# Kernel optimization log

Hardware: AMD Instinct MI355X
Metric: run time of the kernel (lower is better)

Reference implementation:

```python
import jax, jax.numpy as jnp
import numpy as np

S, B, I, H, O = 512, 64, 128, 512, 1


def setup_inputs() -> dict:
    key = jax.random.key(0)
    ks = jax.random.split(key, 12)
    s = 1.0 / np.sqrt(H)
    u = lambda k, shape: jax.random.uniform(k, shape, jnp.float32, -s, s)
    return {
        "inputs": jax.random.normal(ks[0], (S, B, I), jnp.float32),
        # pre nn.RNN (1 layer, tanh)
        "W_ih_pre": u(ks[1], (H, I)),
        "W_hh_pre": u(ks[2], (H, H)),
        "b_ih_pre": u(ks[3], (H,)),
        "b_hh_pre": u(ks[4], (H,)),
        # post nn.RNNCell (input_size=hidden_size)
        "W_ih_post": u(ks[5], (H, H)),
        "W_hh_post": u(ks[6], (H, H)),
        "b_ih_post": u(ks[7], (H,)),
        "b_hh_post": u(ks[8], (H,)),
        # fc head
        "W_fc": u(ks[9], (O, H)),
        "b_fc": u(ks[10], (O,)),
    }


def reference(inputs, W_ih_pre, W_hh_pre, b_ih_pre, b_hh_pre,
              W_ih_post, W_hh_post, b_ih_post, b_hh_post, W_fc, b_fc):
    batch = inputs.shape[1]
    hidden = W_ih_pre.shape[0]
    h0 = jnp.zeros((batch, hidden), inputs.dtype)

    # ---- pre RNN over time (tanh cell), inputs are (S, B, I) ----
    x_proj = jnp.einsum('sbi,hi->sbh', inputs, W_ih_pre) + b_ih_pre

    def pre_step(h, x_t):
        h = jnp.tanh(x_t + h @ W_hh_pre.T + b_hh_pre)
        return h, h

    _, out_pre = jax.lax.scan(pre_step, h0, x_proj)  # (S, B, H)

    # ---- attention loop: exactly `hidden` sequential steps ----
    def attn_step(h, _):
        # dot-prod alignment: sum over feature dim -> (S, B)
        scores = jnp.einsum('sbh,bh->sb', out_pre, h)
        w = jax.nn.softmax(scores, axis=0)          # softmax over seq dim
        ctx = jnp.einsum('sbh,sb->bh', out_pre, w)  # weighted sum -> (B, H)
        h = jnp.tanh(ctx @ W_ih_post.T + b_ih_post + h @ W_hh_post.T + b_hh_post)
        return h, None

    h_post, _ = jax.lax.scan(attn_step, h0, None, length=hidden)
    return h_post @ W_fc.T + b_fc  # (B, O)
```

## Files before the change

### kernel.cpp

```cpp
#include <hip/hip_runtime.h>
#include <math.h>

#define NWG 256
#define NTHR 512
static constexpr int S = 512, B = 64, I = 128, H = 512;

static constexpr size_t OFF_BUF0   = 0;
static constexpr size_t OFF_PCTX   = (size_t)S * B * H;
static constexpr size_t OFF_H3X    = OFF_PCTX + (size_t)64 * 4 * 520;
static constexpr size_t OFF_ACTR   = OFF_H3X + (size_t)64 * 512;
static constexpr size_t OFF_HCTR   = OFF_ACTR + (size_t)64 * 4 * 16;
static constexpr size_t OFF_GFLAGS = OFF_HCTR + (size_t)64 * 4 * 16;
static constexpr size_t OFF_END    = OFF_GFLAGS + (size_t)256 * 16;

typedef float f32x2 __attribute__((ext_vector_type(2)));
typedef float f32x4 __attribute__((ext_vector_type(4)));

__device__ __forceinline__ void st_g1(float* p, float v) {
  asm volatile("global_store_dword %0, %1, off sc0 sc1" :: "v"(p), "v"(v) : "memory");
}
__device__ __forceinline__ void st_g2(float* p, f32x2 v) {
  asm volatile("global_store_dwordx2 %0, %1, off sc0 sc1" :: "v"(p), "v"(v) : "memory");
}
__device__ __forceinline__ void st_gu(unsigned* p, unsigned v) {
  asm volatile("global_store_dword %0, %1, off sc0 sc1" :: "v"(p), "v"(v) : "memory");
}
__device__ __forceinline__ f32x4 ld_g4(const float* p) {
  f32x4 v;
  asm volatile("global_load_dwordx4 %0, %1, off sc0 sc1\n\ts_waitcnt vmcnt(0)"
               : "=&v"(v) : "v"(p) : "memory");
  return v;
}
__device__ __forceinline__ f32x4 ld_g4_reg(const float* p) {
  f32x4 v;
  asm volatile("global_load_dwordx4 %0, %1, off\n\ts_waitcnt vmcnt(0)"
               : "=v"(v) : "v"(p));
  return v;
}
__device__ __forceinline__ void ld_3c(const float* v0, const float* v1, const float* v2,
                                      const float* m0, const float* m1, const float* m2,
                                      float& a, float& b, float& c,
                                      f32x2& x, f32x2& y, f32x2& z) {
  asm volatile("global_load_dword %0, %6, off sc0 sc1\n\t"
               "global_load_dword %1, %7, off sc0 sc1\n\t"
               "global_load_dword %2, %8, off sc0 sc1\n\t"
               "global_load_dwordx2 %3, %9, off sc0 sc1\n\t"
               "global_load_dwordx2 %4, %10, off sc0 sc1\n\t"
               "global_load_dwordx2 %5, %11, off sc0 sc1\n\t"
               "s_waitcnt vmcnt(0)"
               : "=&v"(a), "=&v"(b), "=&v"(c), "=&v"(x), "=&v"(y), "=&v"(z)
               : "v"(v0), "v"(v1), "v"(v2), "v"(m0), "v"(m1), "v"(m2) : "memory");
}
__device__ __forceinline__ void poll3_ge(const unsigned* p0, const unsigned* p1,
                                         const unsigned* p2, unsigned tgt) {
  unsigned a, b, c;
  do {
    asm volatile("global_load_dword %0, %3, off sc0 sc1\n\t"
                 "global_load_dword %1, %4, off sc0 sc1\n\t"
                 "global_load_dword %2, %5, off sc0 sc1\n\t"
                 "s_waitcnt vmcnt(0)"
                 : "=&v"(a), "=&v"(b), "=&v"(c)
                 : "v"(p0), "v"(p1), "v"(p2) : "memory");
  } while (a < tgt || b < tgt || c < tgt);
}
__device__ __forceinline__ void vm_drain() { asm volatile("s_waitcnt vmcnt(0)" ::: "memory"); }

__device__ __forceinline__ void gbar_all(unsigned* gflags, int wg, unsigned gen) {
  __syncthreads();
  if (threadIdx.x == 0)
    __hip_atomic_store(gflags + (size_t)wg * 16, gen, __ATOMIC_RELEASE, __HIP_MEMORY_SCOPE_AGENT);
  if (threadIdx.x < 256) {
    while (__hip_atomic_load(gflags + (size_t)threadIdx.x * 16, __ATOMIC_ACQUIRE,
                             __HIP_MEMORY_SCOPE_AGENT) < gen) {}
  }
  __syncthreads();
}

static constexpr int L_MRG = 0;
static constexpr int L_ML  = 4096;
static constexpr int L_H   = 4112;
static constexpr int L_CTX = 4624;

__global__ __launch_bounds__(NTHR) __attribute__((amdgpu_waves_per_eu(1, 2)))
void attn_fused(
    const float* __restrict__ inputs,
    const float* __restrict__ Wih_pre, const float* __restrict__ Whh_pre,
    const float* __restrict__ bih_pre, const float* __restrict__ bhh_pre,
    const float* __restrict__ Wih_post, const float* __restrict__ Whh_post,
    const float* __restrict__ bih_post, const float* __restrict__ bhh_post,
    const float* __restrict__ Wfc, const float* __restrict__ bfc,
    float* __restrict__ out, float* __restrict__ ws)
{
  float* buf0  = ws + OFF_BUF0;
  float* pctxg = ws + OFF_PCTX;
  float* h3xg  = ws + OFF_H3X;
  unsigned* actrg  = (unsigned*)(ws + OFF_ACTR);
  unsigned* hctrg  = (unsigned*)(ws + OFF_HCTR);
  unsigned* gflags = (unsigned*)(ws + OFF_GFLAGS);

  const int wg   = blockIdx.x;
  const int tid  = threadIdx.x;
  const int lane = tid & 63;
  const int wv   = tid >> 6;
  const int b    = wg & 63;
  const int part = wg >> 6;
  const int q1 = (part + 1) & 3, q2 = (part + 2) & 3, q3 = (part + 3) & 3;

  unsigned* hc_own = hctrg + ((size_t)b * 4 + part) * 16;
  unsigned* hc1 = hctrg + ((size_t)b * 4 + q1) * 16;
  unsigned* hc2 = hctrg + ((size_t)b * 4 + q2) * 16;
  unsigned* hc3 = hctrg + ((size_t)b * 4 + q3) * 16;
  unsigned* ac_own = actrg + ((size_t)b * 4 + part) * 16;
  unsigned* ac1 = actrg + ((size_t)b * 4 + q1) * 16;
  unsigned* ac2 = actrg + ((size_t)b * 4 + q2) * 16;
  unsigned* ac3 = actrg + ((size_t)b * 4 + q3) * 16;

  __shared__ __align__(16) float smem[8192];

  {
    const int h = tid;
    f32x4 Wr[32];
    const f32x4* wrow = (const f32x4*)(Wih_pre + (size_t)h * I);
    #pragma unroll
    for (int c = 0; c < 32; ++c) Wr[c] = wrow[c];
    const float bias = bih_pre[h] + bhh_pre[h];
    const int r0 = wg * 128;
    for (int t2 = 0; t2 < 2; ++t2) {
      __syncthreads();
      const f32x4* src = (const f32x4*)(inputs + (size_t)(r0 + t2 * 64) * I);
      for (int idx = tid; idx < 64 * I / 4; idx += NTHR)
        ((f32x4*)smem)[idx] = src[idx];
      __syncthreads();
      for (int r = 0; r < 64; ++r) {
        const f32x4* arow = (const f32x4*)(smem + r * I);
        float acc0 = 0.f, acc1 = 0.f;
        #pragma unroll
        for (int c = 0; c < 32; c += 2) {
          f32x4 a0 = arow[c], a1 = arow[c + 1];
          acc0 += a0.x * Wr[c].x + a0.y * Wr[c].y + a0.z * Wr[c].z + a0.w * Wr[c].w;
          acc1 += a1.x * Wr[c+1].x + a1.y * Wr[c+1].y + a1.z * Wr[c+1].z + a1.w * Wr[c+1].w;
        }
        buf0[(size_t)(r0 + t2 * 64 + r) * H + h] = acc0 + acc1 + bias;
      }
    }
  }
  gbar_all(gflags, wg, 1u);

  const int j  = part * 128 + (tid >> 2);
  const int kq = tid & 3;
  {
    f32x4 wpre[32];
    const f32x4* wrow = (const f32x4*)(Whh_pre + (size_t)j * H);
    #pragma unroll
    for (int i = 0; i < 32; ++i) wpre[i] = ld_g4_reg((const float*)(wrow + 4 * i + kq));

    float* hst = smem + L_H;
    hst[tid] = 0.f;
    __syncthreads();

    for (int t = 0; t < S; ++t) {
      float* brow = buf0 + ((size_t)t * B + b) * H;
      float xp = brow[j];
      const f32x4* hst4 = (const f32x4*)hst;
      float d = 0.f;
      #pragma unroll
      for (int i = 0; i < 32; ++i) {
        f32x4 hv = hst4[4 * i + kq];
        d += wpre[i].x * hv.x + wpre[i].y * hv.y + wpre[i].z * hv.z + wpre[i].w * hv.w;
      }
      d += __shfl_xor(d, 1);
      d += __shfl_xor(d, 2);
      float hnew = tanhf(xp + d);
      const int par = (t + 1) & 1;
      float* slot = pctxg + (((size_t)b * 2 + par) * 4 + part) * 128;
      if (kq == 0) {
        brow[j] = hnew;
        st_g1(slot + (tid >> 2), hnew);
      }
      vm_drain();
      __syncthreads();
      if (tid == 0) st_gu(hc_own, (unsigned)(t + 1));
      if (wv == 0) poll3_ge(hc1, hc2, hc3, (unsigned)(t + 1));
      __syncthreads();
      if (tid < 128) {
        f32x4 hv = ld_g4(pctxg + (((size_t)b * 2 + par) * 4) * 128 + (size_t)tid * 4);
        ((f32x4*)hst)[tid] = hv;
      }
      __syncthreads();
    }
  }
  gbar_all(gflags, wg, 2u);

  f32x4 ga[16], gb[16];
  {
    const int s0 = part * 128 + wv * 16;
    #pragma unroll
    for (int i = 0; i < 16; ++i) {
      const float* row = buf0 + ((size_t)(s0 + i) * B + b) * H;
      ga[i] = ld_g4_reg(row + lane * 4);
      gb[i] = ld_g4_reg(row + 256 + lane * 4);
    }
  }

  const f32x4* wihr = (const f32x4*)(Wih_post + (size_t)j * H);
  const f32x4* whhr = (const f32x4*)(Whh_post + (size_t)j * H);
  const float bp3 = bih_post[j] + bhh_post[j];

  float* blk_own = pctxg + ((size_t)b * 4 + part) * 520;
  float* blk1 = pctxg + ((size_t)b * 4 + q1) * 520;
  float* blk2 = pctxg + ((size_t)b * 4 + q2) * 520;
  float* blk3 = pctxg + ((size_t)b * 4 + q3) * 520;

  smem[L_H + tid] = 0.f;
  __syncthreads();

  for (int u = 0; u < H; ++u) {
    float mstar, lsum;
    {
      f32x4 h0v = ((const f32x4*)(smem + L_H))[lane];
      f32x4 h1v = ((const f32x4*)(smem + L_H))[64 + lane];
      float p[16];
      #pragma unroll
      for (int i = 0; i < 16; ++i)
        p[i] = ga[i].x * h0v.x + ga[i].y * h0v.y + ga[i].z * h0v.z + ga[i].w * h0v.w
             + gb[i].x * h1v.x + gb[i].y * h1v.y + gb[i].z * h1v.z + gb[i].w * h1v.w;
      #pragma unroll
      for (int off = 32; off > 0; off >>= 1) {
        #pragma unroll
        for (int i = 0; i < 16; ++i) p[i] += __shfl_xor(p[i], off);
      }
      float m = p[0];
      #pragma unroll
      for (int i = 1; i < 16; ++i) m = fmaxf(m, p[i]);
      float l = 0.f;
      f32x4 c0 = {0.f,0.f,0.f,0.f}, c1 = {0.f,0.f,0.f,0.f};
      #pragma unroll
      for (int i = 0; i < 16; ++i) {
        float e = __expf(p[i] - m);
        l += e;
        c0 += e * ga[i];
        c1 += e * gb[i];
      }
      float* ctx_lds = smem + L_MRG;
      float* ml_lds  = smem + L_ML;
      *(f32x4*)(ctx_lds + wv * 512 + lane * 4)       = c0;
      *(f32x4*)(ctx_lds + wv * 512 + 256 + lane * 4) = c1;
      if (lane == 0) { ml_lds[wv * 2] = m; ml_lds[wv * 2 + 1] = l; }
      __syncthreads();
      mstar = ml_lds[0];
      #pragma unroll
      for (int w = 1; w < 8; ++w) mstar = fmaxf(mstar, ml_lds[w * 2]);
      lsum = 0.f;
      float csum = 0.f;
      #pragma unroll
      for (int w = 0; w < 8; ++w) {
        float sc = __expf(ml_lds[w * 2] - mstar);
        lsum += sc * ml_lds[w * 2 + 1];
        csum += sc * ctx_lds[w * 512 + tid];
      }
      smem[L_CTX + tid] = csum;
      st_g1(blk_own + tid, csum);
      if (tid == 0) st_g2(blk_own + 512, f32x2{mstar, lsum});
      vm_drain();
      __syncthreads();
      if (tid == 0) st_gu(ac_own, (unsigned)(u + 1));
    }

    float zacc = 0.f;
    {
      const f32x4* h4 = (const f32x4*)(smem + L_H);
      #pragma unroll
      for (int i = 0; i < 32; ++i) {
        f32x4 w = whhr[4 * i + kq];
        f32x4 hv = h4[4 * i + kq];
        zacc += w.x * hv.x + w.y * hv.y + w.z * hv.z + w.w * hv.w;
      }
    }

    {
      if (wv == 0) poll3_ge(ac1, ac2, ac3, (unsigned)(u + 1));
      __syncthreads();
      float v1, v2, v3; f32x2 mlA, mlB, mlC;
      ld_3c(blk1 + tid, blk2 + tid, blk3 + tid,
            blk1 + 512, blk2 + 512, blk3 + 512, v1, v2, v3, mlA, mlB, mlC);
      float mb = fmaxf(fmaxf(mstar, mlA.x), fmaxf(mlB.x, mlC.x));
      float s0 = __expf(mstar - mb), s1 = __expf(mlA.x - mb);
      float s2 = __expf(mlB.x - mb), s3 = __expf(mlC.x - mb);
      float inv = 1.0f / (s0 * lsum + s1 * mlA.y + s2 * mlB.y + s3 * mlC.y);
      float cval = (s0 * smem[L_CTX + tid] + s1 * v1 + s2 * v2 + s3 * v3) * inv;
      __syncthreads();
      smem[L_CTX + tid] = cval;
      __syncthreads();
      const f32x4* ctx4 = (const f32x4*)(smem + L_CTX);
      float acc = zacc;
      #pragma unroll
      for (int i = 0; i < 32; ++i) {
        f32x4 w = wihr[4 * i + kq];
        f32x4 cv = ctx4[4 * i + kq];
        acc += w.x * cv.x + w.y * cv.y + w.z * cv.z + w.w * cv.w;
      }
      acc += __shfl_xor(acc, 1);
      acc += __shfl_xor(acc, 2);
      float hnew = tanhf(acc + bp3);
      if (kq == 0) st_g1(h3xg + (size_t)b * 512 + part * 128 + (tid >> 2), hnew);
      vm_drain();
      __syncthreads();
      if (tid == 0) st_gu(hc_own, (unsigned)(513 + u));
      if (wv == 0) poll3_ge(hc1, hc2, hc3, (unsigned)(513 + u));
      __syncthreads();
      if (tid < 128) {
        f32x4 hv = ld_g4(h3xg + (size_t)b * 512 + (size_t)tid * 4);
        ((f32x4*)(smem + L_H))[tid] = hv;
      }
      __syncthreads();
    }
  }

  if (part == 0) {
    float pv = smem[L_H + tid] * Wfc[tid];
    #pragma unroll
    for (int off = 32; off > 0; off >>= 1) pv += __shfl_xor(pv, off);
    __syncthreads();
    if (lane == 0) smem[L_ML + wv] = pv;
    __syncthreads();
    if (tid == 0) {
      float s = 0.f;
      #pragma unroll
      for (int w = 0; w < 8; ++w) s += smem[L_ML + w];
      out[b] = s + bfc[0];
    }
  }
}

extern "C" void kernel_launch(void* const* d_in, const int* in_sizes, int n_in,
                              void* d_out, int out_size, void* d_ws, size_t ws_size,
                              hipStream_t stream) {
  (void)in_sizes; (void)n_in; (void)out_size; (void)ws_size;
  const float* inputs   = (const float*)d_in[0];
  const float* Wih_pre  = (const float*)d_in[1];
  const float* Whh_pre  = (const float*)d_in[2];
  const float* bih_pre  = (const float*)d_in[3];
  const float* bhh_pre  = (const float*)d_in[4];
  const float* Wih_post = (const float*)d_in[5];
  const float* Whh_post = (const float*)d_in[6];
  const float* bih_post = (const float*)d_in[7];
  const float* bhh_post = (const float*)d_in[8];
  const float* Wfc      = (const float*)d_in[9];
  const float* bfc      = (const float*)d_in[10];
  float* out = (float*)d_out;
  float* ws  = (float*)d_ws;

  hipMemsetAsync((char*)d_ws + OFF_ACTR * sizeof(float), 0,
                 (OFF_END - OFF_ACTR) * sizeof(float), stream);

  attn_fused<<<dim3(NWG), dim3(NTHR), 0, stream>>>(
      inputs, Wih_pre, Whh_pre, bih_pre, bhh_pre,
      Wih_post, Whh_post, bih_post, bhh_post, Wfc, bfc, out, ws);
}
```

Measured before the change: 13.73 ms.

## Move half of attention keys to LDS and stream half of W_hh_pre from memory

Halves the register-resident attention key rows (ga/gb) and stages the other half in a new 128KB LDS region that is read every attention step. In the pre-RNN loop, only half of the W_hh_pre row is held in registers and the rest is reloaded from global memory each timestep. The aim is to cut VGPR pressure and likely spills. The cost is extra LDS traffic per step, extra global loads in the serial recurrence, and exp values computed twice.

Measured after the change: 17.84 ms. 30.0% more time.

```diff
diff --git a/kernel.cpp b/kernel.cpp
--- a/kernel.cpp
+++ b/kernel.cpp
@@ -34,7 +34,7 @@
 __device__ __forceinline__ f32x4 ld_g4_reg(const float* p) {
   f32x4 v;
   asm volatile("global_load_dwordx4 %0, %1, off\n\ts_waitcnt vmcnt(0)"
-               : "=v"(v) : "v"(p));
+               : "=&v"(v) : "v"(p));
   return v;
 }
 __device__ __forceinline__ void ld_3c(const float* v0, const float* v1, const float* v2,
@@ -76,10 +76,11 @@
   __syncthreads();
 }
 
-static constexpr int L_MRG = 0;
-static constexpr int L_ML  = 4096;
-static constexpr int L_H   = 4112;
-static constexpr int L_CTX = 4624;
+static constexpr int L_G   = 0;
+static constexpr int L_MRG = 32768;
+static constexpr int L_ML  = 36864;
+static constexpr int L_H   = 36880;
+static constexpr int L_CTX = 37392;
 
 __global__ __launch_bounds__(NTHR) __attribute__((amdgpu_waves_per_eu(1, 2)))
 void attn_fused(
@@ -115,7 +116,7 @@
   unsigned* ac2 = actrg + ((size_t)b * 4 + q2) * 16;
   unsigned* ac3 = actrg + ((size_t)b * 4 + q3) * 16;
 
-  __shared__ __align__(16) float smem[8192];
+  __shared__ __align__(16) float smem[37904];
 
   {
     const int h = tid;
@@ -149,10 +150,10 @@
   const int j  = part * 128 + (tid >> 2);
   const int kq = tid & 3;
   {
-    f32x4 wpre[32];
     const f32x4* wrow = (const f32x4*)(Whh_pre + (size_t)j * H);
+    f32x4 wpA[16];
     #pragma unroll
-    for (int i = 0; i < 32; ++i) wpre[i] = ld_g4_reg((const float*)(wrow + 4 * i + kq));
+    for (int i = 0; i < 16; ++i) wpA[i] = ld_g4_reg((const float*)(wrow + 4 * i + kq));
 
     float* hst = smem + L_H;
     hst[tid] = 0.f;
@@ -162,12 +163,19 @@
       float* brow = buf0 + ((size_t)t * B + b) * H;
       float xp = brow[j];
       const f32x4* hst4 = (const f32x4*)hst;
-      float d = 0.f;
-      #pragma unroll
-      for (int i = 0; i < 32; ++i) {
+      float d0 = 0.f, d1 = 0.f;
+      #pragma unroll
+      for (int i = 0; i < 16; ++i) {
         f32x4 hv = hst4[4 * i + kq];
-        d += wpre[i].x * hv.x + wpre[i].y * hv.y + wpre[i].z * hv.z + wpre[i].w * hv.w;
-      }
+        d0 += wpA[i].x * hv.x + wpA[i].y * hv.y + wpA[i].z * hv.z + wpA[i].w * hv.w;
+      }
+      #pragma unroll
+      for (int i = 16; i < 32; ++i) {
+        f32x4 w = wrow[4 * i + kq];
+        f32x4 hv = hst4[4 * i + kq];
+        d1 += w.x * hv.x + w.y * hv.y + w.z * hv.z + w.w * hv.w;
+      }
+      float d = d0 + d1;
       d += __shfl_xor(d, 1);
       d += __shfl_xor(d, 2);
       float hnew = tanhf(xp + d);
@@ -191,16 +199,23 @@
   }
   gbar_all(gflags, wg, 2u);
 
-  f32x4 ga[16], gb[16];
+  f32x4 ga[8], gb[8];
   {
     const int s0 = part * 128 + wv * 16;
     #pragma unroll
-    for (int i = 0; i < 16; ++i) {
+    for (int i = 0; i < 8; ++i) {
       const float* row = buf0 + ((size_t)(s0 + i) * B + b) * H;
       ga[i] = ld_g4_reg(row + lane * 4);
       gb[i] = ld_g4_reg(row + 256 + lane * 4);
     }
-  }
+    for (int idx = tid; idx < 64 * 128; idx += NTHR) {
+      int lr = idx >> 7, c4 = idx & 127;
+      int srow = part * 128 + (lr >> 3) * 16 + 8 + (lr & 7);
+      f32x4 v = *(const f32x4*)(buf0 + ((size_t)srow * B + b) * H + 4 * c4);
+      *(f32x4*)(smem + L_G + lr * 512 + 4 * c4) = v;
+    }
+  }
+  __syncthreads();
 
   const f32x4* wihr = (const f32x4*)(Wih_post + (size_t)j * H);
   const f32x4* whhr = (const f32x4*)(Whh_post + (size_t)j * H);
@@ -221,9 +236,17 @@
       f32x4 h1v = ((const f32x4*)(smem + L_H))[64 + lane];
       float p[16];
       #pragma unroll
-      for (int i = 0; i < 16; ++i)
+      for (int i = 0; i < 8; ++i)
         p[i] = ga[i].x * h0v.x + ga[i].y * h0v.y + ga[i].z * h0v.z + ga[i].w * h0v.w
              + gb[i].x * h1v.x + gb[i].y * h1v.y + gb[i].z * h1v.z + gb[i].w * h1v.w;
+      #pragma unroll
+      for (int i = 0; i < 8; ++i) {
+        const f32x4* lrow = (const f32x4*)(smem + L_G + (wv * 8 + i) * 512);
+        f32x4 g0 = lrow[lane];
+        f32x4 g1 = lrow[64 + lane];
+        p[8 + i] = g0.x * h0v.x + g0.y * h0v.y + g0.z * h0v.z + g0.w * h0v.w
+                 + g1.x * h1v.x + g1.y * h1v.y + g1.z * h1v.z + g1.w * h1v.w;
+      }
       #pragma unroll
       for (int off = 32; off > 0; off >>= 1) {
         #pragma unroll
@@ -235,11 +258,21 @@
       float l = 0.f;
       f32x4 c0 = {0.f,0.f,0.f,0.f}, c1 = {0.f,0.f,0.f,0.f};
       #pragma unroll
-      for (int i = 0; i < 16; ++i) {
+      for (int i = 0; i < 16; ++i) l += __expf(p[i] - m);
+      #pragma unroll
+      for (int i = 0; i < 8; ++i) {
         float e = __expf(p[i] - m);
-        l += e;
         c0 += e * ga[i];
         c1 += e * gb[i];
+      }
+      #pragma unroll
+      for (int i = 0; i < 8; ++i) {
+        float e = __expf(p[8 + i] - m);
+        const f32x4* lrow = (const f32x4*)(smem + L_G + (wv * 8 + i) * 512);
+        f32x4 g0 = lrow[lane];
+        f32x4 g1 = lrow[64 + lane];
+        c0 += e * g0;
+        c1 += e * g1;
       }
       float* ctx_lds = smem + L_MRG;
       float* ml_lds  = smem + L_ML;
```
